# Kernel tuning notes

Hardware: AMD Instinct MI355X
Metric: run time of the kernel (lower is better)

## Reference

```python
import jax, jax.numpy as jnp
import numpy as np

N = 100000      # nodes
E = 3200000     # edges (avg degree 32)
IN = 128        # in_channels
H = 32          # hidden dim
OUT = 64        # out_channels
L = 31          # number of SGConv layers


def setup_inputs() -> dict:
    key = jax.random.key(0)
    ks = jax.random.split(key, 10)
    x = jax.random.normal(ks[0], (N, IN), dtype=jnp.float32)
    edge_index = jax.random.randint(ks[1], (2, E), 0, N, dtype=jnp.int32)
    s = 0.05
    W1 = jax.random.normal(ks[2], (H, IN), dtype=jnp.float32) * s
    b1 = jnp.zeros((H,), dtype=jnp.float32)
    Wc = jax.random.normal(ks[3], (L, H, H), dtype=jnp.float32) * s
    bc = jnp.zeros((L, H), dtype=jnp.float32)
    W32 = jax.random.normal(ks[4], (OUT, 32 * H), dtype=jnp.float32) * s
    b32 = jnp.zeros((OUT,), dtype=jnp.float32)
    return {"x": x, "edge_index": edge_index, "W1": W1, "b1": b1,
            "Wc": Wc, "bc": bc, "W32": W32, "b32": b32}


def mynorm(t):
    # min/max over feature axis (dim=1 of [N, C]; last axis in general)
    mn = jnp.min(t, axis=-1, keepdims=True)
    mx = jnp.max(t, axis=-1, keepdims=True)
    return 2.0 * (t - mn) / (mx - mn + 1e-8) - 1.0


def reference(x, edge_index, W1, b1, Wc, bc, W32, b32):
    n = x.shape[0]
    loops = jnp.arange(n, dtype=edge_index.dtype)
    row = jnp.concatenate([edge_index[0], loops])  # source
    col = jnp.concatenate([edge_index[1], loops])  # target
    # symmetric GCN normalization (PyG gcn_norm, add_self_loops=True)
    deg = jax.ops.segment_sum(jnp.ones_like(row, dtype=x.dtype), col, num_segments=n)
    dis = jnp.where(deg > 0, jax.lax.rsqrt(deg), 0.0)
    nrm = (dis[row] * dis[col])[:, None]  # [E+N, 1]

    def prop(h):
        # out[col] += norm * h[row]
        return jax.ops.segment_sum(h[row] * nrm, col, num_segments=n)

    x0 = mynorm(jax.nn.relu(x @ W1.T + b1))  # [N, 32]

    def step(h, p):
        W, b = p
        y = prop(h) @ W.T + b  # SGConv K=1: propagate then linear
        return y, y

    _, ys = jax.lax.scan(step, x0, (Wc, bc))  # [31, N, 32]
    xs = jnp.concatenate([x0[None], ys], axis=0)  # [32, N, 32]
    m = mynorm(xs)
    # xx1 = x1; xxk = mynorm(xk) - mynorm(x_{k-2}); original uses raw x16 at slot 16
    feats = [x0, xs[1]]
    for k in range(2, 32):
        feats.append(xs[k] if k == 16 else m[k] - m[k - 2])
    cat = jnp.concatenate(feats, axis=1)  # [N, 1024]
    return cat @ W32.T + b32  # [N, 64]
```

## Files before the change

kernel.cpp:

```cpp
#include <hip/hip_runtime.h>
#include <hip/hip_fp16.h>

#define NN 100000
#define NE 3200000
#define NB8 12500

static __device__ __forceinline__ void acc8(float* a, uint4 uu) {
    float2 t;
    t = __half22float2(*(__half2*)&uu.x); a[0] += t.x; a[1] += t.y;
    t = __half22float2(*(__half2*)&uu.y); a[2] += t.x; a[3] += t.y;
    t = __half22float2(*(__half2*)&uu.z); a[4] += t.x; a[5] += t.y;
    t = __half22float2(*(__half2*)&uu.w); a[6] += t.x; a[7] += t.y;
}

__global__ __launch_bounds__(256) void k_deg(const int* __restrict__ col, int* __restrict__ deg) {
    int e = blockIdx.x * 256 + threadIdx.x;
    if (e < NE) atomicAdd(&deg[col[e]], 1);
}

__global__ __launch_bounds__(256) void k_bsum(const int* __restrict__ deg, int* __restrict__ bsum) {
    __shared__ int s[256];
    int t = threadIdx.x, i = blockIdx.x * 256 + t;
    s[t] = (i < NN) ? deg[i] : 0;
    __syncthreads();
    for (int st = 128; st > 0; st >>= 1) {
        if (t < st) s[t] += s[t + st];
        __syncthreads();
    }
    if (t == 0) bsum[blockIdx.x] = s[0];
}

__global__ __launch_bounds__(512) void k_scanb(int* __restrict__ bsum, int nb) {
    __shared__ int s[512];
    int t = threadIdx.x;
    s[t] = (t < nb) ? bsum[t] : 0;
    __syncthreads();
    for (int off = 1; off < 512; off <<= 1) {
        int v = (t >= off) ? s[t - off] : 0;
        __syncthreads();
        s[t] += v;
        __syncthreads();
    }
    if (t < nb) bsum[t] = (t == 0) ? 0 : s[t - 1];
}

__global__ __launch_bounds__(256) void k_colptr(const int* __restrict__ deg, const int* __restrict__ bsum,
                                                int* __restrict__ colptr) {
    __shared__ int s[256];
    int t = threadIdx.x, i = blockIdx.x * 256 + t;
    int v = (i < NN) ? deg[i] : 0;
    s[t] = v;
    __syncthreads();
    for (int off = 1; off < 256; off <<= 1) {
        int u = (t >= off) ? s[t - off] : 0;
        __syncthreads();
        s[t] += u;
        __syncthreads();
    }
    if (i <= NN) colptr[i] = bsum[blockIdx.x] + s[t] - v;
}

__global__ __launch_bounds__(256) void k_dis(int* __restrict__ degdis) {
    int i = blockIdx.x * 256 + threadIdx.x;
    if (i < NN) {
        int d = degdis[i];
        ((float*)degdis)[i] = 1.0f / sqrtf((float)(d + 1));
    }
}

__global__ __launch_bounds__(256) void k_scatter(const int* __restrict__ ei, const int* __restrict__ colptr,
                                                 int* __restrict__ cursor, int* __restrict__ csr_row, int p) {
    int e = blockIdx.x * 256 + threadIdx.x;
    if (e < NE) {
        int c = ei[NE + e];
        int lo = p * NB8;
        if (c >= lo && c < lo + NB8) {
            int r = ei[e];
            int pos = colptr[c] + atomicAdd(&cursor[c], 1);
            csr_row[pos] = r;
        }
    }
}

__global__ __launch_bounds__(256) void k_x0(const float* __restrict__ x, const float* __restrict__ W1,
                                            const float* __restrict__ b1, const float* __restrict__ W32,
                                            const float* __restrict__ b32, const float* __restrict__ dis,
                                            __half* __restrict__ h0, __half* __restrict__ ring0,
                                            float* __restrict__ out, float* __restrict__ Mhat,
                                            float* __restrict__ SCar) {
    __shared__ float sW1[32 * 128];
    __shared__ float sW32[64 * 32];
    __shared__ float sb1[32], sb32[64];
    int t = threadIdx.x;
    if (blockIdx.x == 0 && t == 0) SCar[0] = 1.0f;
    for (int i = t; i < 4096; i += 256) sW1[i] = W1[i];
    for (int i = t; i < 2048; i += 256) sW32[i] = W32[(i >> 5) * 1024 + (i & 31)];
    if (t < 32) sb1[t] = b1[t];
    if (t < 64) sb32[t] = b32[t];
    __syncthreads();
    int node = blockIdx.x * 256 + t;
    if (node >= NN) return;

    float acc[32];
#pragma unroll
    for (int c = 0; c < 32; c++) acc[c] = sb1[c];
    const float4* xr4 = (const float4*)(x + (long)node * 128);
    for (int q = 0; q < 32; q++) {
        float4 xv = xr4[q];
#pragma unroll
        for (int c = 0; c < 32; c++) {
            acc[c] += xv.x * sW1[c * 128 + q * 4] + xv.y * sW1[c * 128 + q * 4 + 1] +
                      xv.z * sW1[c * 128 + q * 4 + 2] + xv.w * sW1[c * 128 + q * 4 + 3];
        }
    }
    float mn = 1e30f, mx = -1e30f;
#pragma unroll
    for (int c = 0; c < 32; c++) {
        acc[c] = fmaxf(acc[c], 0.f);
        mn = fminf(mn, acc[c]);
        mx = fmaxf(mx, acc[c]);
    }
    float inv = 2.f / (mx - mn + 1e-8f);
#pragma unroll
    for (int c = 0; c < 32; c++) acc[c] = inv * (acc[c] - mn) - 1.f;
    float sc = dis[node];
    __half2* hr = (__half2*)(h0 + (long)node * 32);
#pragma unroll
    for (int q = 0; q < 16; q++) hr[q] = __floats2half2_rn(sc * acc[2 * q], sc * acc[2 * q + 1]);
    if (t == 0 && (blockIdx.x & 15) == 0) atomicMax((int*)&Mhat[0], __float_as_int(sc));
    float mn2 = 1e30f, mx2 = -1e30f;
#pragma unroll
    for (int c = 0; c < 32; c++) {
        mn2 = fminf(mn2, acc[c]);
        mx2 = fmaxf(mx2, acc[c]);
    }
    float inv2 = 2.f / (mx2 - mn2 + 1e-8f);
    __half2* rr = (__half2*)(ring0 + (long)node * 32);
#pragma unroll
    for (int q = 0; q < 16; q++)
        rr[q] = __floats2half2_rn(inv2 * (acc[2 * q] - mn2) - 1.f, inv2 * (acc[2 * q + 1] - mn2) - 1.f);
    float* orow = out + (long)node * 64;
    for (int o = 0; o < 64; o++) {
        float a = sb32[o];
#pragma unroll
        for (int j = 0; j < 32; j++) a += sW32[o * 32 + j] * acc[j];
        orow[o] = a;
    }
}

__global__ __launch_bounds__(256, 3) void k_layer(const __half* __restrict__ hin, __half* __restrict__ hout,
                                                  __half* __restrict__ ring, const float* __restrict__ dis,
                                                  const int* __restrict__ colptr, const int* __restrict__ csr_row,
                                                  const float* __restrict__ Wck, const float* __restrict__ bck,
                                                  const float* __restrict__ W32k, float* __restrict__ out,
                                                  float* __restrict__ Mhat, float* __restrict__ SCar, int k,
                                                  int rawfeat) {
    __shared__ float sWc[32 * 33];
    __shared__ float sW[64 * 33];
    __shared__ float sbc[32];
    int t = threadIdx.x;
    float SCin = SCar[k - 1];
    float SCk = SCin * fmaxf(Mhat[k - 1], 1e-30f);
    if (t == 0) SCar[k] = SCk;
    float invSCk = 1.0f / SCk;
    for (int i = t; i < 1024; i += 256) sWc[(i >> 5) * 33 + (i & 31)] = Wck[i];
    for (int i = t; i < 2048; i += 256) sW[(i >> 5) * 33 + (i & 31)] = W32k[(i >> 5) * 1024 + (i & 31)];
    if (t < 32) sbc[t] = bck[t];
    __syncthreads();

    int wave = t >> 6, lane = t & 63;
    int sub = lane >> 2, q = lane & 3;
    int node = blockIdx.x * 64 + wave * 16 + sub;
    if (node >= NN) return;
    int sl = sub * 4;

    const uint4* __restrict__ h4 = (const uint4*)hin;
    int e0 = colptr[node], e1 = colptr[node + 1];
    float di = dis[node];

    float a[8], b[8];
#pragma unroll
    for (int i = 0; i < 8; i++) { a[i] = 0.f; b[i] = 0.f; }
    acc8(a, h4[(long)node * 4 + q]);

    int base = e0;
    while (base + 8 <= e1) {
        int r1v = csr_row[base + q];
        int r2v = csr_row[base + 4 + q];
#pragma unroll
        for (int j = 0; j < 4; j++) {
            int ra = __shfl(r1v, sl + j, 64);
            int rb = __shfl(r2v, sl + j, 64);
            uint4 ua = h4[(long)ra * 4 + q];
            uint4 ub = h4[(long)rb * 4 + q];
            acc8(a, ua);
            acc8(b, ub);
        }
        base += 8;
    }
    int rem = e1 - base;
    if (rem >= 4) {
        int rv = csr_row[base + q];
#pragma unroll
        for (int j = 0; j < 4; j++) {
            int rr = __shfl(rv, sl + j, 64);
            acc8(a, h4[(long)rr * 4 + q]);
        }
        base += 4;
        rem -= 4;
    }
    if (rem > 0) {
        int rv = (q < rem) ? csr_row[base + q] : 0;
        for (int j = 0; j < rem; j++) {
            int rr = __shfl(rv, sl + j, 64);
            acc8(b, h4[(long)rr * 4 + q]);
        }
    }
    float g[8];
#pragma unroll
    for (int i = 0; i < 8; i++) g[i] = di * (a[i] + b[i]);

    float y[8];
#pragma unroll
    for (int i = 0; i < 8; i++) y[i] = 0.f;
#pragma unroll
    for (int s = 0; s < 4; s++) {
        float tv[8];
#pragma unroll
        for (int i = 0; i < 8; i++) tv[i] = __shfl(g[i], sl + s, 64);
        int jb = 8 * s;
#pragma unroll
        for (int i = 0; i < 8; i++) {
            const float* w = &sWc[(8 * q + i) * 33 + jb];
#pragma unroll
            for (int j = 0; j < 8; j++) y[i] += w[j] * tv[j];
        }
    }
#pragma unroll
    for (int i = 0; i < 8; i++) y[i] = SCin * y[i] + sbc[8 * q + i];

    {
        uint4 pw;
        __half2 p0 = __floats2half2_rn(di * y[0] * invSCk, di * y[1] * invSCk);
        __half2 p1 = __floats2half2_rn(di * y[2] * invSCk, di * y[3] * invSCk);
        __half2 p2 = __floats2half2_rn(di * y[4] * invSCk, di * y[5] * invSCk);
        __half2 p3 = __floats2half2_rn(di * y[6] * invSCk, di * y[7] * invSCk);
        pw.x = *(unsigned int*)&p0;
        pw.y = *(unsigned int*)&p1;
        pw.z = *(unsigned int*)&p2;
        pw.w = *(unsigned int*)&p3;
        ((uint4*)hout)[(long)node * 4 + q] = pw;
    }

    float mn = y[0], mx = y[0];
#pragma unroll
    for (int i = 1; i < 8; i++) {
        mn = fminf(mn, y[i]);
        mx = fmaxf(mx, y[i]);
    }
    mn = fminf(mn, __shfl_xor(mn, 1, 64));
    mn = fminf(mn, __shfl_xor(mn, 2, 64));
    mx = fmaxf(mx, __shfl_xor(mx, 1, 64));
    mx = fmaxf(mx, __shfl_xor(mx, 2, 64));
    float inv = 2.f / (mx - mn + 1e-8f);
    float mv[8];
#pragma unroll
    for (int i = 0; i < 8; i++) mv[i] = inv * (y[i] - mn) - 1.f;

    if ((blockIdx.x & 15) == 0 && q == 0) {
        float rowmax = fmaxf(fabsf(mn), fabsf(mx));
        atomicMax((int*)&Mhat[k], __float_as_int(di * rowmax * invSCk));
    }

    float f[8];
    if (rawfeat) {
#pragma unroll
        for (int i = 0; i < 8; i++) f[i] = y[i];
    } else {
        uint4 rv = ((const uint4*)ring)[(long)node * 4 + q];
        float rr[8];
        float2 tt;
        tt = __half22float2(*(__half2*)&rv.x); rr[0] = tt.x; rr[1] = tt.y;
        tt = __half22float2(*(__half2*)&rv.y); rr[2] = tt.x; rr[3] = tt.y;
        tt = __half22float2(*(__half2*)&rv.z); rr[4] = tt.x; rr[5] = tt.y;
        tt = __half22float2(*(__half2*)&rv.w); rr[6] = tt.x; rr[7] = tt.y;
#pragma unroll
        for (int i = 0; i < 8; i++) f[i] = mv[i] - rr[i];
    }
    {
        uint4 pw;
        __half2 p0 = __floats2half2_rn(mv[0], mv[1]);
        __half2 p1 = __floats2half2_rn(mv[2], mv[3]);
        __half2 p2 = __floats2half2_rn(mv[4], mv[5]);
        __half2 p3 = __floats2half2_rn(mv[6], mv[7]);
        pw.x = *(unsigned int*)&p0;
        pw.y = *(unsigned int*)&p1;
        pw.z = *(unsigned int*)&p2;
        pw.w = *(unsigned int*)&p3;
        ((uint4*)ring)[(long)node * 4 + q] = pw;
    }

    float o[16];
#pragma unroll
    for (int i = 0; i < 16; i++) o[i] = 0.f;
#pragma unroll
    for (int s = 0; s < 4; s++) {
        float tv[8];
#pragma unroll
        for (int i = 0; i < 8; i++) tv[i] = __shfl(f[i], sl + s, 64);
        int jb = 8 * s;
#pragma unroll
        for (int i = 0; i < 16; i++) {
            const float* w = &sW[(16 * q + i) * 33 + jb];
#pragma unroll
            for (int j = 0; j < 8; j++) o[i] += w[j] * tv[j];
        }
    }
    float4* op = (float4*)(out + (long)node * 64 + 16 * q);
#pragma unroll
    for (int i = 0; i < 4; i++) {
        float4 v = op[i];
        v.x += o[4 * i + 0];
        v.y += o[4 * i + 1];
        v.z += o[4 * i + 2];
        v.w += o[4 * i + 3];
        op[i] = v;
    }
}

extern "C" void kernel_launch(void* const* d_in, const int* in_sizes, int n_in, void* d_out, int out_size,
                              void* d_ws, size_t ws_size, hipStream_t stream) {
    const float* x = (const float*)d_in[0];
    const int* ei = (const int*)d_in[1];
    const float* W1 = (const float*)d_in[2];
    const float* b1 = (const float*)d_in[3];
    const float* Wc = (const float*)d_in[4];
    const float* bc = (const float*)d_in[5];
    const float* W32 = (const float*)d_in[6];
    const float* b32 = (const float*)d_in[7];
    float* out = (float*)d_out;

    uintptr_t base = ((uintptr_t)d_ws + 255) & ~(uintptr_t)255;
    __half* h0 = (__half*)base;
    __half* h1 = h0 + (long)NN * 32;
    __half* ring = h1 + (long)NN * 32;
    int* deg = (int*)(ring + (long)2 * NN * 32);
    int* cursor = deg + NN;
    float* Mhat = (float*)(cursor + NN);
    float* SCar = Mhat + 64;
    int* colptr = (int*)(SCar + 64);
    int* bsum = colptr + 100004;
    int* csr_row = bsum + 1024;
    float* dis = (float*)deg;

    hipMemsetAsync(deg, 0, (2 * NN + 128) * sizeof(int), stream);
    k_deg<<<(NE + 255) / 256, 256, 0, stream>>>(ei + NE, deg);
    int NB = (NN + 255) / 256;
    k_bsum<<<NB, 256, 0, stream>>>(deg, bsum);
    k_scanb<<<1, 512, 0, stream>>>(bsum, NB);
    k_colptr<<<NB, 256, 0, stream>>>(deg, bsum, colptr);
    k_dis<<<(NN + 255) / 256, 256, 0, stream>>>(deg);
    for (int p = 0; p < 8; p++)
        k_scatter<<<(NE + 255) / 256, 256, 0, stream>>>(ei, colptr, cursor, csr_row, p);
    k_x0<<<NB, 256, 0, stream>>>(x, W1, b1, W32, b32, dis, h0, ring, out, Mhat, SCar);

    for (int k = 1; k <= 31; k++) {
        const __half* hin = (k & 1) ? h0 : h1;
        __half* hout = (k & 1) ? h1 : h0;
        __half* ringk = ring + (long)(k & 1) * NN * 32;
        int raw = (k == 1 || k == 16) ? 1 : 0;
        k_layer<<<(NN + 63) / 64, 256, 0, stream>>>(hin, hout, ringk, dis, colptr, csr_row, Wc + (k - 1) * 1024,
                                                    bc + (k - 1) * 32, W32 + 32 * k, out, Mhat, SCar, k, raw);
    }
}
```

Measured before the change: 2.642 ms.

## Split node features into two half-width planes and gather each in separate kernels

Hidden state is stored as two 16-channel fp16 planes instead of one 32-channel array. Each layer now runs two gather passes: one over the low half, writing a partial result to a scratch buffer, and one over the high half that also applies the linear layer, norm and output update. Each gathered plane is 3.2 MB instead of 6.4 MB, so it is more likely to stay in L2/LLC during the random gather. In exchange, the CSR indices are read twice per layer, there are twice as many launches, and the scratch buffer adds extra traffic. Nontemporal stores are also used for the outputs.

```diff
diff --git a/kernel.cpp b/kernel.cpp
--- a/kernel.cpp
+++ b/kernel.cpp
@@ -5,12 +5,13 @@
 #define NE 3200000
 #define NB8 12500
 
-static __device__ __forceinline__ void acc8(float* a, uint4 uu) {
-    float2 t;
-    t = __half22float2(*(__half2*)&uu.x); a[0] += t.x; a[1] += t.y;
-    t = __half22float2(*(__half2*)&uu.y); a[2] += t.x; a[3] += t.y;
-    t = __half22float2(*(__half2*)&uu.z); a[4] += t.x; a[5] += t.y;
-    t = __half22float2(*(__half2*)&uu.w); a[6] += t.x; a[7] += t.y;
+typedef unsigned int uint2v __attribute__((ext_vector_type(2)));
+typedef unsigned int uint4v __attribute__((ext_vector_type(4)));
+
+static __device__ __forceinline__ void acc4(float* a, uint2 u) {
+    float2 lo = __half22float2(*(__half2*)&u.x);
+    float2 hi = __half22float2(*(__half2*)&u.y);
+    a[0] += lo.x; a[1] += lo.y; a[2] += hi.x; a[3] += hi.y;
 }
 
 __global__ __launch_bounds__(256) void k_deg(const int* __restrict__ col, int* __restrict__ deg) {
@@ -85,9 +86,9 @@
 __global__ __launch_bounds__(256) void k_x0(const float* __restrict__ x, const float* __restrict__ W1,
                                             const float* __restrict__ b1, const float* __restrict__ W32,
                                             const float* __restrict__ b32, const float* __restrict__ dis,
-                                            __half* __restrict__ h0, __half* __restrict__ ring0,
-                                            float* __restrict__ out, float* __restrict__ Mhat,
-                                            float* __restrict__ SCar) {
+                                            __half* __restrict__ hlo, __half* __restrict__ hhi,
+                                            __half* __restrict__ ring0, float* __restrict__ out,
+                                            float* __restrict__ Mhat, float* __restrict__ SCar) {
     __shared__ float sW1[32 * 128];
     __shared__ float sW32[64 * 32];
     __shared__ float sb1[32], sb32[64];
@@ -124,9 +125,13 @@
 #pragma unroll
     for (int c = 0; c < 32; c++) acc[c] = inv * (acc[c] - mn) - 1.f;
     float sc = dis[node];
-    __half2* hr = (__half2*)(h0 + (long)node * 32);
-#pragma unroll
-    for (int q = 0; q < 16; q++) hr[q] = __floats2half2_rn(sc * acc[2 * q], sc * acc[2 * q + 1]);
+    __half2* hl = (__half2*)(hlo + (long)node * 16);
+    __half2* hh = (__half2*)(hhi + (long)node * 16);
+#pragma unroll
+    for (int q = 0; q < 8; q++) {
+        hl[q] = __floats2half2_rn(sc * acc[2 * q], sc * acc[2 * q + 1]);
+        hh[q] = __floats2half2_rn(sc * acc[16 + 2 * q], sc * acc[16 + 2 * q + 1]);
+    }
     if (t == 0 && (blockIdx.x & 15) == 0) atomicMax((int*)&Mhat[0], __float_as_int(sc));
     float mn2 = 1e30f, mx2 = -1e30f;
 #pragma unroll
@@ -148,13 +153,70 @@
     }
 }
 
-__global__ __launch_bounds__(256, 3) void k_layer(const __half* __restrict__ hin, __half* __restrict__ hout,
-                                                  __half* __restrict__ ring, const float* __restrict__ dis,
-                                                  const int* __restrict__ colptr, const int* __restrict__ csr_row,
-                                                  const float* __restrict__ Wck, const float* __restrict__ bck,
-                                                  const float* __restrict__ W32k, float* __restrict__ out,
-                                                  float* __restrict__ Mhat, float* __restrict__ SCar, int k,
-                                                  int rawfeat) {
+__global__ __launch_bounds__(256) void k_ga(const __half* __restrict__ hlo, __half* __restrict__ glo,
+                                            const int* __restrict__ colptr, const int* __restrict__ csr_row) {
+    int t = threadIdx.x;
+    int wave = t >> 6, lane = t & 63;
+    int sub = lane >> 2, q = lane & 3;
+    int node = blockIdx.x * 64 + wave * 16 + sub;
+    if (node >= NN) return;
+    int sl = sub * 4;
+
+    const uint2* __restrict__ h2 = (const uint2*)hlo;
+    int e0 = colptr[node], e1 = colptr[node + 1];
+
+    float a[4] = {0.f, 0.f, 0.f, 0.f}, b[4] = {0.f, 0.f, 0.f, 0.f};
+    acc4(a, h2[(long)node * 4 + q]);
+
+    int base = e0;
+    while (base + 8 <= e1) {
+        int r1 = csr_row[base + q];
+        int r2 = csr_row[base + 4 + q];
+#pragma unroll
+        for (int j = 0; j < 4; j++) {
+            int ra = __shfl(r1, sl + j, 64);
+            int rb = __shfl(r2, sl + j, 64);
+            uint2 ua = h2[(long)ra * 4 + q];
+            uint2 ub = h2[(long)rb * 4 + q];
+            acc4(a, ua);
+            acc4(b, ub);
+        }
+        base += 8;
+    }
+    int rem = e1 - base;
+    if (rem >= 4) {
+        int rv = csr_row[base + q];
+#pragma unroll
+        for (int j = 0; j < 4; j++) {
+            int rr = __shfl(rv, sl + j, 64);
+            acc4(a, h2[(long)rr * 4 + q]);
+        }
+        base += 4;
+        rem -= 4;
+    }
+    if (rem > 0) {
+        int rv = (q < rem) ? csr_row[base + q] : 0;
+        for (int j = 0; j < rem; j++) {
+            int rr = __shfl(rv, sl + j, 64);
+            acc4(b, h2[(long)rr * 4 + q]);
+        }
+    }
+    __half2 p0 = __floats2half2_rn(a[0] + b[0], a[1] + b[1]);
+    __half2 p1 = __floats2half2_rn(a[2] + b[2], a[3] + b[3]);
+    uint2v pw;
+    pw.x = *(unsigned int*)&p0;
+    pw.y = *(unsigned int*)&p1;
+    __builtin_nontemporal_store(pw, (uint2v*)((uint2*)glo + (long)node * 4 + q));
+}
+
+__global__ __launch_bounds__(256, 3) void k_gb(const __half* __restrict__ hhi, const __half* __restrict__ glo,
+                                               __half* __restrict__ hlo_out, __half* __restrict__ hhi_out,
+                                               __half* __restrict__ ring, const float* __restrict__ dis,
+                                               const int* __restrict__ colptr, const int* __restrict__ csr_row,
+                                               const float* __restrict__ Wck, const float* __restrict__ bck,
+                                               const float* __restrict__ W32k, float* __restrict__ out,
+                                               float* __restrict__ Mhat, float* __restrict__ SCar, int k,
+                                               int rawfeat) {
     __shared__ float sWc[32 * 33];
     __shared__ float sW[64 * 33];
     __shared__ float sbc[32];
@@ -174,27 +236,25 @@
     if (node >= NN) return;
     int sl = sub * 4;
 
-    const uint4* __restrict__ h4 = (const uint4*)hin;
+    const uint2* __restrict__ h2 = (const uint2*)hhi;
     int e0 = colptr[node], e1 = colptr[node + 1];
     float di = dis[node];
 
-    float a[8], b[8];
-#pragma unroll
-    for (int i = 0; i < 8; i++) { a[i] = 0.f; b[i] = 0.f; }
-    acc8(a, h4[(long)node * 4 + q]);
+    float a[4] = {0.f, 0.f, 0.f, 0.f}, b[4] = {0.f, 0.f, 0.f, 0.f};
+    acc4(a, h2[(long)node * 4 + q]);
 
     int base = e0;
     while (base + 8 <= e1) {
-        int r1v = csr_row[base + q];
-        int r2v = csr_row[base + 4 + q];
+        int r1 = csr_row[base + q];
+        int r2 = csr_row[base + 4 + q];
 #pragma unroll
         for (int j = 0; j < 4; j++) {
-            int ra = __shfl(r1v, sl + j, 64);
-            int rb = __shfl(r2v, sl + j, 64);
-            uint4 ua = h4[(long)ra * 4 + q];
-            uint4 ub = h4[(long)rb * 4 + q];
-            acc8(a, ua);
-            acc8(b, ub);
+            int ra = __shfl(r1, sl + j, 64);
+            int rb = __shfl(r2, sl + j, 64);
+            uint2 ua = h2[(long)ra * 4 + q];
+            uint2 ub = h2[(long)rb * 4 + q];
+            acc4(a, ua);
+            acc4(b, ub);
         }
         base += 8;
     }
@@ -204,7 +264,7 @@
 #pragma unroll
         for (int j = 0; j < 4; j++) {
             int rr = __shfl(rv, sl + j, 64);
-            acc8(a, h4[(long)rr * 4 + q]);
+            acc4(a, h2[(long)rr * 4 + q]);
         }
         base += 4;
         rem -= 4;
@@ -213,43 +273,54 @@
         int rv = (q < rem) ? csr_row[base + q] : 0;
         for (int j = 0; j < rem; j++) {
             int rr = __shfl(rv, sl + j, 64);
-            acc8(b, h4[(long)rr * 4 + q]);
-        }
-    }
-    float g[8];
-#pragma unroll
-    for (int i = 0; i < 8; i++) g[i] = di * (a[i] + b[i]);
+            acc4(b, h2[(long)rr * 4 + q]);
+        }
+    }
+    float gA[4], gB[4];
+    {
+        uint2 u = ((const uint2*)glo)[(long)node * 4 + q];
+        float2 lo = __half22float2(*(__half2*)&u.x);
+        float2 hi = __half22float2(*(__half2*)&u.y);
+        gA[0] = di * lo.x; gA[1] = di * lo.y; gA[2] = di * hi.x; gA[3] = di * hi.y;
+    }
+#pragma unroll
+    for (int j = 0; j < 4; j++) gB[j] = di * (a[j] + b[j]);
 
     float y[8];
 #pragma unroll
     for (int i = 0; i < 8; i++) y[i] = 0.f;
 #pragma unroll
     for (int s = 0; s < 4; s++) {
-        float tv[8];
-#pragma unroll
-        for (int i = 0; i < 8; i++) tv[i] = __shfl(g[i], sl + s, 64);
-        int jb = 8 * s;
+        float ta[4], tb[4];
+#pragma unroll
+        for (int j = 0; j < 4; j++) {
+            ta[j] = __shfl(gA[j], sl + s, 64);
+            tb[j] = __shfl(gB[j], sl + s, 64);
+        }
 #pragma unroll
         for (int i = 0; i < 8; i++) {
-            const float* w = &sWc[(8 * q + i) * 33 + jb];
-#pragma unroll
-            for (int j = 0; j < 8; j++) y[i] += w[j] * tv[j];
+            const float* w = &sWc[(8 * q + i) * 33];
+#pragma unroll
+            for (int j = 0; j < 4; j++) y[i] += w[4 * s + j] * ta[j] + w[16 + 4 * s + j] * tb[j];
         }
     }
 #pragma unroll
     for (int i = 0; i < 8; i++) y[i] = SCin * y[i] + sbc[8 * q + i];
 
     {
-        uint4 pw;
         __half2 p0 = __floats2half2_rn(di * y[0] * invSCk, di * y[1] * invSCk);
         __half2 p1 = __floats2half2_rn(di * y[2] * invSCk, di * y[3] * invSCk);
         __half2 p2 = __floats2half2_rn(di * y[4] * invSCk, di * y[5] * invSCk);
         __half2 p3 = __floats2half2_rn(di * y[6] * invSCk, di * y[7] * invSCk);
+        uint4v pw;
         pw.x = *(unsigned int*)&p0;
         pw.y = *(unsigned int*)&p1;
         pw.z = *(unsigned int*)&p2;
         pw.w = *(unsigned int*)&p3;
-        ((uint4*)hout)[(long)node * 4 + q] = pw;
+        if (q < 2)
+            __builtin_nontemporal_store(pw, (uint4v*)((uint4*)hlo_out + (long)node * 2 + q));
+        else
+            __builtin_nontemporal_store(pw, (uint4v*)((uint4*)hhi_out + (long)node * 2 + (q - 2)));
     }
 
     float mn = y[0], mx = y[0];
@@ -278,21 +349,21 @@
         for (int i = 0; i < 8; i++) f[i] = y[i];
     } else {
         uint4 rv = ((const uint4*)ring)[(long)node * 4 + q];
-        float rr[8];
-        float2 tt;
-        tt = __half22float2(*(__half2*)&rv.x); rr[0] = tt.x; rr[1] = tt.y;
-        tt = __half22float2(*(__half2*)&rv.y); rr[2] = tt.x; rr[3] = tt.y;
-        tt = __half22float2(*(__half2*)&rv.z); rr[4] = tt.x; rr[5] = tt.y;
-        tt = __half22float2(*(__half2*)&rv.w); rr[6] = tt.x; rr[7] = tt.y;
-#pragma unroll
-        for (int i = 0; i < 8; i++) f[i] = mv[i] - rr[i];
+        float2 t0 = __half22float2(*(__half2*)&rv.x);
+        float2 t1 = __half22float2(*(__half2*)&rv.y);
+        float2 t2 = __half22float2(*(__half2*)&rv.z);
+        float2 t3 = __half22float2(*(__half2*)&rv.w);
+        f[0] = mv[0] - t0.x; f[1] = mv[1] - t0.y;
+        f[2] = mv[2] - t1.x; f[3] = mv[3] - t1.y;
+        f[4] = mv[4] - t2.x; f[5] = mv[5] - t2.y;
+        f[6] = mv[6] - t3.x; f[7] = mv[7] - t3.y;
     }
     {
-        uint4 pw;
         __half2 p0 = __floats2half2_rn(mv[0], mv[1]);
         __half2 p1 = __floats2half2_rn(mv[2], mv[3]);
         __half2 p2 = __floats2half2_rn(mv[4], mv[5]);
         __half2 p3 = __floats2half2_rn(mv[6], mv[7]);
+        uint4 pw;
         pw.x = *(unsigned int*)&p0;
         pw.y = *(unsigned int*)&p1;
         pw.z = *(unsigned int*)&p2;
@@ -305,15 +376,14 @@
     for (int i = 0; i < 16; i++) o[i] = 0.f;
 #pragma unroll
     for (int s = 0; s < 4; s++) {
-        float tv[8];
-#pragma unroll
-        for (int i = 0; i < 8; i++) tv[i] = __shfl(f[i], sl + s, 64);
-        int jb = 8 * s;
+        float tf[8];
+#pragma unroll
+        for (int j = 0; j < 8; j++) tf[j] = __shfl(f[j], sl + s, 64);
 #pragma unroll
         for (int i = 0; i < 16; i++) {
-            const float* w = &sW[(16 * q + i) * 33 + jb];
-#pragma unroll
-            for (int j = 0; j < 8; j++) o[i] += w[j] * tv[j];
+            const float* w = &sW[(16 * q + i) * 33 + 8 * s];
+#pragma unroll
+            for (int j = 0; j < 8; j++) o[i] += w[j] * tf[j];
         }
     }
     float4* op = (float4*)(out + (long)node * 64 + 16 * q);
@@ -341,9 +411,12 @@
     float* out = (float*)d_out;
 
     uintptr_t base = ((uintptr_t)d_ws + 255) & ~(uintptr_t)255;
-    __half* h0 = (__half*)base;
-    __half* h1 = h0 + (long)NN * 32;
-    __half* ring = h1 + (long)NN * 32;
+    __half* hlo0 = (__half*)base;
+    __half* hlo1 = hlo0 + (long)NN * 16;
+    __half* hhi0 = hlo1 + (long)NN * 16;
+    __half* hhi1 = hhi0 + (long)NN * 16;
+    __half* glo = hhi1 + (long)NN * 16;
+    __half* ring = glo + (long)NN * 16;
     int* deg = (int*)(ring + (long)2 * NN * 32);
     int* cursor = deg + NN;
     float* Mhat = (float*)(cursor + NN);
@@ -362,14 +435,19 @@
     k_dis<<<(NN + 255) / 256, 256, 0, stream>>>(deg);
     for (int p = 0; p < 8; p++)
         k_scatter<<<(NE + 255) / 256, 256, 0, stream>>>(ei, colptr, cursor, csr_row, p);
-    k_x0<<<NB, 256, 0, stream>>>(x, W1, b1, W32, b32, dis, h0, ring, out, Mhat, SCar);
-
+    k_x0<<<NB, 256, 0, stream>>>(x, W1, b1, W32, b32, dis, hlo0, hhi0, ring, out, Mhat, SCar);
+
+    int NBL = (NN + 63) / 64;
     for (int k = 1; k <= 31; k++) {
-        const __half* hin = (k & 1) ? h0 : h1;
-        __half* hout = (k & 1) ? h1 : h0;
+        const __half* hinlo = (k & 1) ? hlo0 : hlo1;
+        const __half* hinhi = (k & 1) ? hhi0 : hhi1;
+        __half* houtlo = (k & 1) ? hlo1 : hlo0;
+        __half* houthi = (k & 1) ? hhi1 : hhi0;
         __half* ringk = ring + (long)(k & 1) * NN * 32;
         int raw = (k == 1 || k == 16) ? 1 : 0;
-        k_layer<<<(NN + 63) / 64, 256, 0, stream>>>(hin, hout, ringk, dis, colptr, csr_row, Wc + (k - 1) * 1024,
-                                                    bc + (k - 1) * 32, W32 + 32 * k, out, Mhat, SCar, k, raw);
-    }
-}
+        k_ga<<<NBL, 256, 0, stream>>>(hinlo, glo, colptr, csr_row);
+        k_gb<<<NBL, 256, 0, stream>>>(hinhi, glo, houtlo, houthi, ringk, dis, colptr, csr_row,
+                                      Wc + (k - 1) * 1024, bc + (k - 1) * 32, W32 + 32 * k, out, Mhat, SCar, k,
+                                      raw);
+    }
+}
```

New measurement: 3.232 ms. +22.3%, slower.
